# Kernel tuning notes

Hardware: AMD Instinct MI355X
Metric: run time of the kernel (lower is better)

## Reference

```python
import jax, jax.numpy as jnp
import numpy as np

N, E, G = 50000, 800000, 64
H, C = 4, 32            # heads, per-head channels
IN, ED = 128, 16        # in_channels, edge_dim
NEG_SLOPE = 0.2


def gat_conv(x, edge_index, edge_attr, W, att_src, att_dst, W_e, att_e, bias, concat):
    """PyG GATConv (eval mode, add_self_loops=True, fill_value='mean').
    x: [N,F_in], edge_index: [2,E], edge_attr: [E,ED].
    W: [F_in,H*C], att_*: [H,C], W_e: [ED,H*C], bias: [H*C] or [C].
    """
    n = x.shape[0]
    # add self loops; self-loop edge_attr = mean of edge_attr (fill_value='mean')
    loop = jnp.arange(n, dtype=edge_index.dtype)
    src = jnp.concatenate([edge_index[0], loop])
    dst = jnp.concatenate([edge_index[1], loop])
    ea = jnp.concatenate(
        [edge_attr, jnp.broadcast_to(edge_attr.mean(0), (n, edge_attr.shape[1]))], 0)

    xw = (x @ W).reshape(n, H, C)                       # [N,H,C]
    a_src = (xw * att_src).sum(-1)                      # [N,H]
    a_dst = (xw * att_dst).sum(-1)                      # [N,H]
    ew = (ea @ W_e).reshape(-1, H, C)                   # [E+N,H,C]
    a_edge = (ew * att_e).sum(-1)                       # [E+N,H]

    alpha = a_src[src] + a_dst[dst] + a_edge            # [E+N,H]
    alpha = jax.nn.leaky_relu(alpha, NEG_SLOPE)
    # segment softmax over incoming edges of each dst node
    amax = jax.ops.segment_max(alpha, dst, num_segments=n)
    alpha = jnp.exp(alpha - amax[dst])
    denom = jax.ops.segment_sum(alpha, dst, num_segments=n)
    alpha = alpha / (denom[dst] + 1e-16)

    msg = alpha[:, :, None] * xw[src]                   # [E+N,H,C]
    out = jax.ops.segment_sum(msg, dst, num_segments=n) # [N,H,C]
    out = out.reshape(n, H * C) if concat else out.mean(1)
    return out + bias


def setup_inputs() -> dict:
    key = jax.random.key(0)
    ks = jax.random.split(key, 24)
    g = lambda i, shape, scale=0.1: jax.random.normal(ks[i], shape, jnp.float32) * scale
    inp = {
        "x": jax.random.normal(ks[0], (N, IN), jnp.float32),
        "edge_index": jax.random.randint(ks[1], (2, E), 0, N, jnp.int64 if jax.config.jax_enable_x64 else jnp.int32),
        "edge_attr": jax.random.normal(ks[2], (E, ED), jnp.float32),
        "batch": jnp.sort(jax.random.randint(ks[3], (N,), 0, G)),
        # conv1: in=128 -> H*C=128, concat
        "W1": g(4, (IN, H * C)), "att_src1": g(5, (H, C)), "att_dst1": g(6, (H, C)),
        "W_e1": g(7, (ED, H * C)), "att_e1": g(8, (H, C)), "b1": g(9, (H * C,)),
        # conv2: in=H*C=128 -> C=32, mean over heads
        "W2": g(10, (H * C, H * C)), "att_src2": g(11, (H, C)), "att_dst2": g(12, (H, C)),
        "W_e2": g(13, (ED, H * C)), "att_e2": g(14, (H, C)), "b2": g(15, (C,)),
        # graph MLP: 32 -> 32 -> 2
        "W3": g(16, (C, C)), "b3": g(17, (C,)),
        "W4": g(18, (C, 2)), "b4": g(19, (2,)),
    }
    return inp


def reference(x, edge_index, edge_attr, batch,
              W1, att_src1, att_dst1, W_e1, att_e1, b1,
              W2, att_src2, att_dst2, W_e2, att_e2, b2,
              W3, b3, W4, b4):
    h = gat_conv(x, edge_index, edge_attr, W1, att_src1, att_dst1, W_e1, att_e1, b1, concat=True)
    h = jax.nn.relu(h)   # dropout inactive in eval mode
    h = gat_conv(h, edge_index, edge_attr, W2, att_src2, att_dst2, W_e2, att_e2, b2, concat=False)
    # global mean pool over graphs
    sums = jax.ops.segment_sum(h, batch, num_segments=G)            # [G,C]
    cnt = jax.ops.segment_sum(jnp.ones((h.shape[0], 1), h.dtype), batch, num_segments=G)
    pooled = sums / jnp.maximum(cnt, 1.0)
    out = jax.nn.relu(pooled @ W3 + b3) @ W4 + b4                   # [G,2]
    return out
```

## Files before the change

### kernel.cpp

```cpp
#include <hip/hip_runtime.h>
#include <hip/hip_bf16.h>

#define NEG_SLOPE 0.2f
#define BINB 512
#define BIN_CHUNK 2048
#define MAXBKT 2048

typedef __attribute__((ext_vector_type(8))) short bf16x8;
typedef __attribute__((ext_vector_type(4))) float f32x4;

__device__ __forceinline__ unsigned short bf16rne(float x) {
    unsigned int u = __float_as_uint(x);
    u += 0x7fffu + ((u >> 16) & 1u);
    return (unsigned short)(u >> 16);
}
__device__ __forceinline__ unsigned int pk2bf16(float lo, float hi) {
    return ((unsigned int)bf16rne(hi) << 16) | bf16rne(lo);
}

__global__ void init_kernel(int* __restrict__ bucket_cnt, float* __restrict__ ea_sums,
                            float* __restrict__ pooled) {
    int t = threadIdx.x;
    for (int i = t; i < BINB; i += 256) bucket_cnt[i] = 0;
    if (t < 16) ea_sums[t] = 0.f;
    for (int i = t; i < 2048; i += 256) pooled[i] = 0.f;
}

__global__ __launch_bounds__(256) void ea_colsum(const float* __restrict__ ea,
                                                 float* __restrict__ sums, int E_) {
    int j = threadIdx.x & 15, rl = threadIdx.x >> 4;
    float acc = 0.f;
    for (long long r = (long long)blockIdx.x * 16 + rl; r < E_; r += (long long)gridDim.x * 16)
        acc += ea[r * 16 + j];
    __shared__ float red[256];
    red[rl * 16 + j] = acc;
    __syncthreads();
    if (threadIdx.x < 16) {
        float s = 0.f;
#pragma unroll
        for (int i = 0; i < 16; i++) s += red[i * 16 + threadIdx.x];
        atomicAdd(&sums[threadIdx.x], s);
    }
}

__global__ __launch_bounds__(256) void bin_count(const int* __restrict__ dst,
                                                 int* __restrict__ bucket_cnt,
                                                 int* __restrict__ blockbase,
                                                 int E_, int EN_, int npb) {
    __shared__ int hist[BINB];
    int tid = threadIdx.x;
    for (int i = tid; i < BINB; i += 256) hist[i] = 0;
    __syncthreads();
    int base = blockIdx.x * BIN_CHUNK;
    int lim = min(base + BIN_CHUNK, EN_);
    for (int e = base + tid; e < lim; e += 256) {
        int d = (e < E_) ? dst[e] : e - E_;
        atomicAdd(&hist[d / npb], 1);
    }
    __syncthreads();
    for (int b = tid; b < BINB; b += 256) {
        int c = hist[b];
        blockbase[blockIdx.x * BINB + b] = (c > 0) ? atomicAdd(&bucket_cnt[b], c) : 0;
    }
}

__global__ __launch_bounds__(512) void bucket_scan(const int* __restrict__ bucket_cnt,
                                                   int* __restrict__ bucket_off,
                                                   int* __restrict__ rowptr, int n, int total) {
    __shared__ int tmp[BINB];
    int t = threadIdx.x;
    tmp[t] = bucket_cnt[t];
    __syncthreads();
    for (int off = 1; off < BINB; off <<= 1) {
        int v = (t >= off) ? tmp[t - off] : 0;
        __syncthreads();
        tmp[t] += v;
        __syncthreads();
    }
    bucket_off[t] = (t == 0) ? 0 : tmp[t - 1];
    if (t == 0) rowptr[n] = total;
}

__global__ __launch_bounds__(256) void bin_scatter(const int* __restrict__ src,
                                                   const int* __restrict__ dst,
                                                   const int* __restrict__ bucket_off,
                                                   const int* __restrict__ blockbase,
                                                   int2* __restrict__ bin_se,
                                                   int E_, int EN_, int npb) {
    __shared__ int hist[BINB];
    int tid = threadIdx.x;
    for (int i = tid; i < BINB; i += 256) hist[i] = 0;
    __syncthreads();
    int base = blockIdx.x * BIN_CHUNK;
    int lim = min(base + BIN_CHUNK, EN_);
    for (int e = base + tid; e < lim; e += 256) {
        int s, d;
        if (e < E_) { s = src[e]; d = dst[e]; } else { s = d = e - E_; }
        int b = d / npb;
        int rank = atomicAdd(&hist[b], 1);
        int pos = bucket_off[b] + blockbase[blockIdx.x * BINB + b] + rank;
        bin_se[pos] = make_int2(s, e | ((d - b * npb) << 20));
    }
}

__global__ __launch_bounds__(256) void csr_build(const int* __restrict__ bucket_off,
                                                 const int2* __restrict__ bin_se,
                                                 int2* __restrict__ csr_se,
                                                 int* __restrict__ row_of,
                                                 int* __restrict__ rowptr,
                                                 int n, int EN_, int npb) {
    __shared__ int pk[MAXBKT];
    __shared__ int sv[MAXBKT];
    __shared__ int cnts[256];
    int b = blockIdx.x;
    int tid = threadIdx.x;
    int nb = b * npb;
    int nn = min(npb, n - nb);
    if (nn <= 0) return;
    int off0 = bucket_off[b];
    int off1 = (b == BINB - 1) ? EN_ : bucket_off[b + 1];
    int cnt = min(off1 - off0, MAXBKT);
    cnts[tid] = 0;
    __syncthreads();
    for (int i = tid; i < cnt; i += 256) {
        int2 se = bin_se[off0 + i];
        sv[i] = se.x;
        pk[i] = se.y;
        atomicAdd(&cnts[se.y >> 20], 1);
    }
    __syncthreads();
    for (int off = 1; off < 256; off <<= 1) {
        int v = (tid >= off) ? cnts[tid - off] : 0;
        __syncthreads();
        cnts[tid] += v;
        __syncthreads();
    }
    int excl = (tid == 0) ? 0 : cnts[tid - 1];
    __syncthreads();
    cnts[tid] = off0 + excl;
    if (tid < nn) rowptr[nb + tid] = off0 + excl;
    __syncthreads();
    for (int i = tid; i < cnt; i += 256) {
        int y = pk[i];
        int dloc = y >> 20;
        int pos = atomicAdd(&cnts[dloc], 1);
        csr_se[pos] = make_int2(sv[i], y & 0xFFFFF);
        row_of[pos] = nb + dloc;
    }
}

__global__ __launch_bounds__(256) void wprep(
    const float* __restrict__ W1, const float* __restrict__ W2,
    const float* __restrict__ We1, const float* __restrict__ ate1,
    const float* __restrict__ We2, const float* __restrict__ ate2,
    const float* __restrict__ ea_sums, float invE,
    unsigned short* __restrict__ Wt1, unsigned short* __restrict__ Wt2,
    float* __restrict__ V1, float* __restrict__ V2,
    float* __restrict__ aes1, float* __restrict__ aes2,
    const int* __restrict__ batch, int* __restrict__ gstart, int n) {
    int b = blockIdx.x, tid = threadIdx.x;
    if (b < 64) {
        const float* W = (b < 32) ? W1 : W2;
        unsigned short* Wt = (b < 32) ? Wt1 : Wt2;
        int base = (b & 31) * 512;
#pragma unroll
        for (int r = 0; r < 2; r++) {
            int flat = base + r * 256 + tid;
            int nn = flat >> 7, k = flat & 127;
            Wt[nn * 128 + k] = bf16rne(W[k * 128 + nn]);
        }
    } else if (b == 64) {
        __shared__ float V1s[64], V2s[64];
        if (tid < 64) {
            int dd = tid >> 2, h = tid & 3;
            float s = 0.f;
            for (int c = 0; c < 32; c++) s += We1[dd * 128 + h * 32 + c] * ate1[h * 32 + c];
            V1[dd * 4 + h] = s; V1s[dd * 4 + h] = s;
        } else if (tid < 128) {
            int t = tid - 64, dd = t >> 2, h = t & 3;
            float s = 0.f;
            for (int c = 0; c < 32; c++) s += We2[dd * 128 + h * 32 + c] * ate2[h * 32 + c];
            V2[dd * 4 + h] = s; V2s[dd * 4 + h] = s;
        }
        __syncthreads();
        if (tid < 4) {
            float s = 0.f;
            for (int dd = 0; dd < 16; dd++) s += ea_sums[dd] * invE * V1s[dd * 4 + tid];
            aes1[tid] = s;
        } else if (tid >= 64 && tid < 68) {
            int h = tid - 64;
            float s = 0.f;
            for (int dd = 0; dd < 16; dd++) s += ea_sums[dd] * invE * V2s[dd * 4 + h];
            aes2[h] = s;
        }
    } else {
        int g = tid;
        if (g > 64) return;
        if (g == 64) { gstart[64] = n; return; }
        int lo = 0, hi = n;
        while (lo < hi) {
            int mid = (lo + hi) >> 1;
            if (batch[mid] < g) lo = mid + 1; else hi = mid;
        }
        gstart[g] = lo;
    }
}

template<bool BF16IN>
__global__ __launch_bounds__(256) void gemm_att_mfma(
    const void* __restrict__ Xin, const unsigned short* __restrict__ Wtg,
    const float* __restrict__ att_s, const float* __restrict__ att_d,
    unsigned short* __restrict__ XWb, float* __restrict__ a_s,
    float* __restrict__ a_d, int n) {
    __shared__ unsigned short Wt[128][136];
    __shared__ unsigned short Xs[4][16][136];
    __shared__ float attsL[128], attdL[128];

    int tid = threadIdx.x;
    int w = tid >> 6, lane = tid & 63;
    int l15 = lane & 15, rgrp = lane >> 4;

    if (tid < 128) { attsL[tid] = att_s[tid]; attdL[tid] = att_d[tid]; }

#pragma unroll
    for (int it = 0; it < 8; it++) {
        int flat = it * 256 + tid;
        int nn = flat >> 4, kq = flat & 15;
        *(uint4*)&Wt[nn][kq * 8] = *(const uint4*)(Wtg + nn * 128 + kq * 8);
    }

    int r0 = blockIdx.x * 64 + w * 16;
    {
        int rr = lane >> 2;
        int row = r0 + rr;
        int c0 = (lane & 3) * 32;
        if (!BF16IN) {
            const float* Xf = (const float*)Xin;
#pragma unroll
            for (int q = 0; q < 8; q++) {
                int c = c0 + q * 4;
                float4 v = make_float4(0.f, 0.f, 0.f, 0.f);
                if (row < n) v = *(const float4*)(Xf + (size_t)row * 128 + c);
                uint2 p;
                p.x = pk2bf16(v.x, v.y);
                p.y = pk2bf16(v.z, v.w);
                *(uint2*)&Xs[w][rr][c] = p;
            }
        } else {
            const unsigned short* Xb = (const unsigned short*)Xin;
#pragma unroll
            for (int q = 0; q < 4; q++) {
                int c = c0 + q * 8;
                uint4 v = make_uint4(0u, 0u, 0u, 0u);
                if (row < n) v = *(const uint4*)(Xb + (size_t)row * 128 + c);
                *(uint4*)&Xs[w][rr][c] = v;
            }
        }
    }
    __syncthreads();

    f32x4 acc[8];
#pragma unroll
    for (int ct = 0; ct < 8; ct++) acc[ct] = (f32x4){0.f, 0.f, 0.f, 0.f};

#pragma unroll
    for (int kt = 0; kt < 4; kt++) {
        int k0 = kt * 32 + rgrp * 8;
        bf16x8 a = *(const bf16x8*)&Xs[w][l15][k0];
#pragma unroll
        for (int ct = 0; ct < 8; ct++) {
            bf16x8 b = *(const bf16x8*)&Wt[ct * 16 + l15][k0];
            acc[ct] = __builtin_amdgcn_mfma_f32_16x16x32_bf16(a, b, acc[ct], 0, 0, 0);
        }
    }

    float ar[8], br[8];
#pragma unroll
    for (int ct = 0; ct < 8; ct++) {
        ar[ct] = attsL[ct * 16 + l15];
        br[ct] = attdL[ct * 16 + l15];
    }
#pragma unroll
    for (int i = 0; i < 4; i++) {
        float ps[4], pd[4];
#pragma unroll
        for (int h = 0; h < 4; h++) {
            ps[h] = acc[2 * h][i] * ar[2 * h] + acc[2 * h + 1][i] * ar[2 * h + 1];
            pd[h] = acc[2 * h][i] * br[2 * h] + acc[2 * h + 1][i] * br[2 * h + 1];
        }
#pragma unroll
        for (int off = 1; off < 16; off <<= 1) {
#pragma unroll
            for (int h = 0; h < 4; h++) {
                ps[h] += __shfl_xor(ps[h], off);
                pd[h] += __shfl_xor(pd[h], off);
            }
        }
        if (l15 == 0) {
            int row = r0 + rgrp * 4 + i;
            if (row < n) {
                *(float4*)(a_s + (size_t)row * 4) = make_float4(ps[0], ps[1], ps[2], ps[3]);
                *(float4*)(a_d + (size_t)row * 4) = make_float4(pd[0], pd[1], pd[2], pd[3]);
            }
        }
    }

    unsigned short* stage = &Xs[w][0][0];
#pragma unroll
    for (int i = 0; i < 4; i++) {
        int row = rgrp * 4 + i;
#pragma unroll
        for (int ct = 0; ct < 8; ct++)
            stage[row * 128 + ct * 16 + l15] = bf16rne(acc[ct][i]);
    }
#pragma unroll
    for (int p = 0; p < 4; p++) {
        int fo = p * 1024 + lane * 16;
        int row = fo >> 8;
        int colb = fo & 255;
        uint4 v = *(const uint4*)((const char*)stage + fo);
        int grow = r0 + row;
        if (grow < n)
            *(uint4*)((char*)XWb + (size_t)grow * 256 + colb) = v;
    }
}

__global__ __launch_bounds__(256) void alpha1_fused(
    const int2* __restrict__ csr_se, const int* __restrict__ row_of,
    const float* __restrict__ ea,
    const float* __restrict__ V1, const float* __restrict__ V2,
    const float* __restrict__ aes1, const float* __restrict__ aes2,
    const float* __restrict__ a_s, const float* __restrict__ a_d,
    float* __restrict__ csr_alpha, float* __restrict__ aeb2, int E_, int EN_) {
    __shared__ float V1l[64], V2l[64], a1l[4], a2l[4];
    int tid = threadIdx.x;
    if (tid < 64) { V1l[tid] = V1[tid]; V2l[tid] = V2[tid]; }
    if (tid < 4) { a1l[tid] = aes1[tid]; a2l[tid] = aes2[tid]; }
    __syncthreads();
    int i = blockIdx.x * 256 + tid;
    if (i >= EN_) return;
    int2 se = csr_se[i];
    int s = se.x, e = se.y, d = row_of[i];
    float ae1[4], ae2[4];
    if (e < E_) {
#pragma unroll
        for (int h = 0; h < 4; h++) { ae1[h] = 0.f; ae2[h] = 0.f; }
        const float4* er = (const float4*)(ea + (size_t)e * 16);
#pragma unroll
        for (int q = 0; q < 4; q++) {
            float4 v = er[q];
#pragma unroll
            for (int h = 0; h < 4; h++) {
                ae1[h] += v.x * V1l[(q * 4 + 0) * 4 + h] + v.y * V1l[(q * 4 + 1) * 4 + h] +
                          v.z * V1l[(q * 4 + 2) * 4 + h] + v.w * V1l[(q * 4 + 3) * 4 + h];
                ae2[h] += v.x * V2l[(q * 4 + 0) * 4 + h] + v.y * V2l[(q * 4 + 1) * 4 + h] +
                          v.z * V2l[(q * 4 + 2) * 4 + h] + v.w * V2l[(q * 4 + 3) * 4 + h];
            }
        }
    } else {
#pragma unroll
        for (int h = 0; h < 4; h++) { ae1[h] = a1l[h]; ae2[h] = a2l[h]; }
    }
    float4 asv = *(const float4*)(a_s + (size_t)s * 4);
    float4 adv = *(const float4*)(a_d + (size_t)d * 4);
    float o0 = asv.x + adv.x + ae1[0];
    float o1 = asv.y + adv.y + ae1[1];
    float o2 = asv.z + adv.z + ae1[2];
    float o3 = asv.w + adv.w + ae1[3];
    o0 = o0 > 0.f ? o0 : NEG_SLOPE * o0;
    o1 = o1 > 0.f ? o1 : NEG_SLOPE * o1;
    o2 = o2 > 0.f ? o2 : NEG_SLOPE * o2;
    o3 = o3 > 0.f ? o3 : NEG_SLOPE * o3;
    *(float4*)(csr_alpha + (size_t)i * 4) = make_float4(o0, o1, o2, o3);
    *(float4*)(aeb2 + (size_t)i * 4) = make_float4(ae2[0], ae2[1], ae2[2], ae2[3]);
}

template<int MODE>
__global__ __launch_bounds__(256) void dst_aggregate(
    const int* __restrict__ rowptr, const int2* __restrict__ csr_se,
    const float* __restrict__ alpha_arr, const float* __restrict__ as2,
    const float* __restrict__ ad2, const uint2* __restrict__ XW2,
    const float* __restrict__ bias, unsigned int* __restrict__ OUT, int n) {
    int wv = threadIdx.x >> 6, lane = threadIdx.x & 63;
    int d = blockIdx.x * 4 + wv;
    if (d >= n) return;
    int h = lane >> 4, j = lane & 15;
    int half = lane >> 5, u = lane & 31;
    int hc16 = (u >> 3) << 4;
    int beg = rowptr[d], end = rowptr[d + 1];

    float advh = 0.f;
    if (MODE == 0) advh = ad2[(size_t)d * 4 + h];

    float a0 = 0.f, a1 = 0.f, a2 = 0.f, a3 = 0.f;
    float den = 0.f;

    int i = beg;
    for (; i + 16 <= end; i += 16) {
        int i0 = i + j;
        int sreg = csr_se[i0].x;
        float a = alpha_arr[(size_t)i0 * 4 + h];
        if (MODE == 0) {
            a += as2[(size_t)sreg * 4 + h] + advh;
            a = a > 0.f ? a : NEG_SLOPE * a;
        }
        float w = __expf(a);
        den += w;
#pragma unroll
        for (int m = 0; m < 8; m++) {
            int k = 2 * m + half;
            int s = __shfl(sreg, k);
            float wk = __shfl(w, hc16 + k);
            uint2 v = XW2[(size_t)s * 32 + u];
            a0 += wk * __uint_as_float(v.x << 16);
            a1 += wk * __uint_as_float(v.x & 0xffff0000u);
            a2 += wk * __uint_as_float(v.y << 16);
            a3 += wk * __uint_as_float(v.y & 0xffff0000u);
        }
    }
    int cnt = end - i;
    if (cnt > 0) {
        float w = 0.f; int sreg = 0;
        if (j < cnt) {
            int i0 = i + j;
            sreg = csr_se[i0].x;
            float a = alpha_arr[(size_t)i0 * 4 + h];
            if (MODE == 0) {
                a += as2[(size_t)sreg * 4 + h] + advh;
                a = a > 0.f ? a : NEG_SLOPE * a;
            }
            w = __expf(a);
        }
        den += w;
        for (int k0 = 0; k0 < cnt; k0 += 4) {
#pragma unroll
            for (int mm = 0; mm < 2; mm++) {
                int k = k0 + 2 * mm + half;
                int kc = k & 15;
                int s = __shfl(sreg, kc);
                float wk = __shfl(w, hc16 + kc);
                if (k >= cnt) wk = 0.f;
                uint2 v = XW2[(size_t)s * 32 + u];
                a0 += wk * __uint_as_float(v.x << 16);
                a1 += wk * __uint_as_float(v.x & 0xffff0000u);
                a2 += wk * __uint_as_float(v.y << 16);
                a3 += wk * __uint_as_float(v.y & 0xffff0000u);
            }
        }
    }
    a0 += __shfl_xor(a0, 32);
    a1 += __shfl_xor(a1, 32);
    a2 += __shfl_xor(a2, 32);
    a3 += __shfl_xor(a3, 32);
    den += __shfl_xor(den, 1);
    den += __shfl_xor(den, 2);
    den += __shfl_xor(den, 4);
    den += __shfl_xor(den, 8);
    float denc = __shfl(den, hc16);
    float inv = 1.f / (denc + 1e-16f);
    if (half == 0) {
        int c0 = u * 4;
        float o0 = a0 * inv, o1 = a1 * inv, o2 = a2 * inv, o3 = a3 * inv;
        if (MODE == 1) {
            float4 bb = *(const float4*)(bias + c0);
            o0 = fmaxf(o0 + bb.x, 0.f);
            o1 = fmaxf(o1 + bb.y, 0.f);
            o2 = fmaxf(o2 + bb.z, 0.f);
            o3 = fmaxf(o3 + bb.w, 0.f);
        }
        uint2 pv;
        pv.x = pk2bf16(o0, o1);
        pv.y = pk2bf16(o2, o3);
        *((uint2*)OUT + (size_t)d * 32 + u) = pv;
    }
}

#define POOL_SPLITS 8
__global__ __launch_bounds__(256) void pool_kernel(const unsigned int* __restrict__ B,
                                                   const int* __restrict__ gstart,
                                                   float* __restrict__ pooled) {
    int g = blockIdx.x / POOL_SPLITS, sp = blockIdx.x % POOL_SPLITS;
    int lo = gstart[g], hi = gstart[g + 1];
    int cnt = hi - lo;
    int per = (cnt + POOL_SPLITS - 1) / POOL_SPLITS;
    int s0 = lo + sp * per;
    int s1 = min(s0 + per, hi);
    int jj = threadIdx.x & 15, rl = threadIdx.x >> 4;
    float ax = 0.f, ay = 0.f;
    for (int node = s0 + rl; node < s1; node += 16) {
        const unsigned int* r = B + (size_t)node * 64;
#pragma unroll
        for (int h = 0; h < 4; h++) {
            unsigned int v = r[h * 16 + jj];
            ax += __uint_as_float(v << 16);
            ay += __uint_as_float(v & 0xffff0000u);
        }
    }
    __shared__ float redx[16][16], redy[16][16];
    redx[rl][jj] = ax * 0.25f;
    redy[rl][jj] = ay * 0.25f;
    __syncthreads();
    if (threadIdx.x < 16) {
        float sx = 0.f, sy = 0.f;
#pragma unroll
        for (int i = 0; i < 16; i++) { sx += redx[i][threadIdx.x]; sy += redy[i][threadIdx.x]; }
        atomicAdd(&pooled[g * 32 + 2 * threadIdx.x], sx);
        atomicAdd(&pooled[g * 32 + 2 * threadIdx.x + 1], sy);
    }
}

__global__ void mlp_kernel(const float* __restrict__ pooled, const int* __restrict__ gstart,
                           const float* __restrict__ b2,
                           const float* __restrict__ W3, const float* __restrict__ b3,
                           const float* __restrict__ W4, const float* __restrict__ b4,
                           float* __restrict__ out) {
    int g = blockIdx.x;
    int c = threadIdx.x;
    __shared__ float pm[32];
    __shared__ float t[32];
    int cnt = gstart[g + 1] - gstart[g];
    if (c < 32) {
        float m = 0.f;
        if (cnt > 0) m = pooled[g * 32 + c] / (float)cnt + b2[c];
        pm[c] = m;
    }
    __syncthreads();
    if (c < 32) {
        float s = b3[c];
        for (int k = 0; k < 32; k++) s += pm[k] * W3[k * 32 + c];
        t[c] = fmaxf(s, 0.f);
    }
    __syncthreads();
    if (c < 2) {
        float o = b4[c];
        for (int k = 0; k < 32; k++) o += t[k] * W4[k * 2 + c];
        out[g * 2 + c] = o;
    }
}

extern "C" void kernel_launch(void* const* d_in, const int* in_sizes, int n_in,
                              void* d_out, int out_size, void* d_ws, size_t ws_size,
                              hipStream_t stream) {
    const float* x    = (const float*)d_in[0];
    const int*   eidx = (const int*)d_in[1];
    const float* ea   = (const float*)d_in[2];
    const int*   batch= (const int*)d_in[3];
    const float* W1   = (const float*)d_in[4];
    const float* as1  = (const float*)d_in[5];
    const float* ad1  = (const float*)d_in[6];
    const float* We1  = (const float*)d_in[7];
    const float* ate1 = (const float*)d_in[8];
    const float* b1   = (const float*)d_in[9];
    const float* W2   = (const float*)d_in[10];
    const float* as2  = (const float*)d_in[11];
    const float* ad2  = (const float*)d_in[12];
    const float* We2  = (const float*)d_in[13];
    const float* ate2 = (const float*)d_in[14];
    const float* b2   = (const float*)d_in[15];
    const float* W3   = (const float*)d_in[16];
    const float* b3   = (const float*)d_in[17];
    const float* W4   = (const float*)d_in[18];
    const float* b4   = (const float*)d_in[19];

    const int N_ = in_sizes[0] / 128;
    const int E_ = in_sizes[1] / 2;
    const int EN = E_ + N_;
    const int* srcp = eidx;
    const int* dstp = eidx + E_;
    const int npb = (N_ + BINB - 1) / BINB;
    const int nbk = (EN + BIN_CHUNK - 1) / BIN_CHUNK;

    char* w = (char*)d_ws;
    size_t off = 0;
    auto alloc = [&](size_t bytes) -> void* {
        void* p = w + off;
        off = (off + bytes + 255) & ~(size_t)255;
        return p;
    };
    unsigned short* A   = (unsigned short*)alloc((size_t)N_ * 128 * 2);
    unsigned short* Bb16= (unsigned short*)alloc((size_t)N_ * 128 * 2);
    float* csr_alpha = (float*)alloc((size_t)EN * 16);
    float* aeb2      = (float*)alloc((size_t)EN * 16);
    int2*  csr_se    = (int2*)alloc((size_t)EN * 8);
    int*   row_of    = (int*)alloc((size_t)EN * 4);
    int2*  bin_se    = (int2*)alloc((size_t)EN * 8);
    int*   rowptr    = (int*)alloc((size_t)(N_ + 1) * 4);
    int*   bucket_cnt= (int*)alloc(BINB * 4);
    int*   bucket_off= (int*)alloc(BINB * 4);
    int*   blockbase = (int*)alloc((size_t)nbk * BINB * 4);
    unsigned short* Wt1g = (unsigned short*)alloc(16384 * 2);
    unsigned short* Wt2g = (unsigned short*)alloc(16384 * 2);
    float* a_s       = (float*)alloc((size_t)N_ * 16);
    float* a_d       = (float*)alloc((size_t)N_ * 16);
    float* ea_sums   = (float*)alloc(64);
    float* V1        = (float*)alloc(256);
    float* V2        = (float*)alloc(256);
    float* aes1      = (float*)alloc(16);
    float* aes2      = (float*)alloc(16);
    float* pooled    = (float*)alloc(64 * 32 * 4);
    int*   gstart    = (int*)alloc(65 * 4);

    init_kernel<<<1, 256, 0, stream>>>(bucket_cnt, ea_sums, pooled);
    ea_colsum<<<1024, 256, 0, stream>>>(ea, ea_sums, E_);
    bin_count<<<nbk, 256, 0, stream>>>(dstp, bucket_cnt, blockbase, E_, EN, npb);
    bucket_scan<<<1, BINB, 0, stream>>>(bucket_cnt, bucket_off, rowptr, N_, EN);
    wprep<<<66, 256, 0, stream>>>(W1, W2, We1, ate1, We2, ate2, ea_sums,
                                  1.0f / (float)E_, Wt1g, Wt2g, V1, V2, aes1, aes2,
                                  batch, gstart, N_);
    bin_scatter<<<nbk, 256, 0, stream>>>(srcp, dstp, bucket_off, blockbase,
                                         bin_se, E_, EN, npb);
    csr_build<<<BINB, 256, 0, stream>>>(bucket_off, bin_se,
                                        csr_se, row_of, rowptr, N_, EN, npb);

    int gblk = (N_ + 63) / 64;

    gemm_att_mfma<false><<<gblk, 256, 0, stream>>>(x, Wt1g, as1, ad1, A, a_s, a_d, N_);
    alpha1_fused<<<(EN + 255) / 256, 256, 0, stream>>>(csr_se, row_of, ea, V1, V2,
                                                       aes1, aes2, a_s, a_d,
                                                       csr_alpha, aeb2, E_, EN);
    dst_aggregate<1><<<(N_ + 3) / 4, 256, 0, stream>>>(rowptr, csr_se, csr_alpha,
                                                       nullptr, nullptr,
                                                       (const uint2*)A, b1,
                                                       (unsigned int*)Bb16, N_);

    gemm_att_mfma<true><<<gblk, 256, 0, stream>>>(Bb16, Wt2g, as2, ad2, A, a_s, a_d, N_);
    dst_aggregate<0><<<(N_ + 3) / 4, 256, 0, stream>>>(rowptr, csr_se, aeb2,
                                                       a_s, a_d,
                                                       (const uint2*)A, b2,
                                                       (unsigned int*)Bb16, N_);
    pool_kernel<<<64 * POOL_SPLITS, 256, 0, stream>>>((const unsigned int*)Bb16,
                                                      gstart, pooled);

    mlp_kernel<<<64, 64, 0, stream>>>(pooled, gstart, b2, W3, b3, W4, b4, (float*)d_out);
}
```

Baseline: 225.4 us.

## Split CSR src/edge arrays and store per-edge attention logits in bf16

The interleaved int2 (src, edge) CSR array becomes two separate int arrays, so the aggregation kernels read only the source indices. The per-edge layer-1 logits and layer-2 edge terms are now stored as packed bf16 (8 bytes per edge instead of 16) and unpacked to float inside dst_aggregate. This cuts edge-stream traffic in alpha1_fused and both aggregation passes. The cost is bf16 rounding of the attention logits before the softmax exponent, which could shift results slightly.

Result: slower. 234.2 us (+3.9%).

```diff
diff --git a/kernel.cpp b/kernel.cpp
--- a/kernel.cpp
+++ b/kernel.cpp
@@ -105,7 +105,8 @@
 
 __global__ __launch_bounds__(256) void csr_build(const int* __restrict__ bucket_off,
                                                  const int2* __restrict__ bin_se,
-                                                 int2* __restrict__ csr_se,
+                                                 int* __restrict__ csr_s,
+                                                 int* __restrict__ csr_e,
                                                  int* __restrict__ row_of,
                                                  int* __restrict__ rowptr,
                                                  int n, int EN_, int npb) {
@@ -144,7 +145,8 @@
         int y = pk[i];
         int dloc = y >> 20;
         int pos = atomicAdd(&cnts[dloc], 1);
-        csr_se[pos] = make_int2(sv[i], y & 0xFFFFF);
+        csr_s[pos] = sv[i];
+        csr_e[pos] = y & 0xFFFFF;
         row_of[pos] = nb + dloc;
     }
 }
@@ -326,12 +328,12 @@
 }
 
 __global__ __launch_bounds__(256) void alpha1_fused(
-    const int2* __restrict__ csr_se, const int* __restrict__ row_of,
-    const float* __restrict__ ea,
+    const int* __restrict__ csr_s, const int* __restrict__ csr_e,
+    const int* __restrict__ row_of, const float* __restrict__ ea,
     const float* __restrict__ V1, const float* __restrict__ V2,
     const float* __restrict__ aes1, const float* __restrict__ aes2,
     const float* __restrict__ a_s, const float* __restrict__ a_d,
-    float* __restrict__ csr_alpha, float* __restrict__ aeb2, int E_, int EN_) {
+    uint2* __restrict__ csr_alpha, uint2* __restrict__ aeb2, int E_, int EN_) {
     __shared__ float V1l[64], V2l[64], a1l[4], a2l[4];
     int tid = threadIdx.x;
     if (tid < 64) { V1l[tid] = V1[tid]; V2l[tid] = V2[tid]; }
@@ -339,8 +341,7 @@
     __syncthreads();
     int i = blockIdx.x * 256 + tid;
     if (i >= EN_) return;
-    int2 se = csr_se[i];
-    int s = se.x, e = se.y, d = row_of[i];
+    int s = csr_s[i], e = csr_e[i], d = row_of[i];
     float ae1[4], ae2[4];
     if (e < E_) {
 #pragma unroll
@@ -371,14 +372,20 @@
     o1 = o1 > 0.f ? o1 : NEG_SLOPE * o1;
     o2 = o2 > 0.f ? o2 : NEG_SLOPE * o2;
     o3 = o3 > 0.f ? o3 : NEG_SLOPE * o3;
-    *(float4*)(csr_alpha + (size_t)i * 4) = make_float4(o0, o1, o2, o3);
-    *(float4*)(aeb2 + (size_t)i * 4) = make_float4(ae2[0], ae2[1], ae2[2], ae2[3]);
+    uint2 pa;
+    pa.x = pk2bf16(o0, o1);
+    pa.y = pk2bf16(o2, o3);
+    csr_alpha[i] = pa;
+    uint2 pe;
+    pe.x = pk2bf16(ae2[0], ae2[1]);
+    pe.y = pk2bf16(ae2[2], ae2[3]);
+    aeb2[i] = pe;
 }
 
 template<int MODE>
 __global__ __launch_bounds__(256) void dst_aggregate(
-    const int* __restrict__ rowptr, const int2* __restrict__ csr_se,
-    const float* __restrict__ alpha_arr, const float* __restrict__ as2,
+    const int* __restrict__ rowptr, const int* __restrict__ csr_s,
+    const unsigned int* __restrict__ alpha_b, const float* __restrict__ as2,
     const float* __restrict__ ad2, const uint2* __restrict__ XW2,
     const float* __restrict__ bias, unsigned int* __restrict__ OUT, int n) {
     int wv = threadIdx.x >> 6, lane = threadIdx.x & 63;
@@ -387,6 +394,7 @@
     int h = lane >> 4, j = lane & 15;
     int half = lane >> 5, u = lane & 31;
     int hc16 = (u >> 3) << 4;
+    int hsel = h >> 1, hodd = h & 1;
     int beg = rowptr[d], end = rowptr[d + 1];
 
     float advh = 0.f;
@@ -398,8 +406,9 @@
     int i = beg;
     for (; i + 16 <= end; i += 16) {
         int i0 = i + j;
-        int sreg = csr_se[i0].x;
-        float a = alpha_arr[(size_t)i0 * 4 + h];
+        int sreg = csr_s[i0];
+        unsigned int au = alpha_b[(size_t)i0 * 2 + hsel];
+        float a = __uint_as_float(hodd ? (au & 0xffff0000u) : (au << 16));
         if (MODE == 0) {
             a += as2[(size_t)sreg * 4 + h] + advh;
             a = a > 0.f ? a : NEG_SLOPE * a;
@@ -423,8 +432,9 @@
         float w = 0.f; int sreg = 0;
         if (j < cnt) {
             int i0 = i + j;
-            sreg = csr_se[i0].x;
-            float a = alpha_arr[(size_t)i0 * 4 + h];
+            sreg = csr_s[i0];
+            unsigned int au = alpha_b[(size_t)i0 * 2 + hsel];
+            float a = __uint_as_float(hodd ? (au & 0xffff0000u) : (au << 16));
             if (MODE == 0) {
                 a += as2[(size_t)sreg * 4 + h] + advh;
                 a = a > 0.f ? a : NEG_SLOPE * a;
@@ -579,9 +589,10 @@
     };
     unsigned short* A   = (unsigned short*)alloc((size_t)N_ * 128 * 2);
     unsigned short* Bb16= (unsigned short*)alloc((size_t)N_ * 128 * 2);
-    float* csr_alpha = (float*)alloc((size_t)EN * 16);
-    float* aeb2      = (float*)alloc((size_t)EN * 16);
-    int2*  csr_se    = (int2*)alloc((size_t)EN * 8);
+    uint2* csr_alpha = (uint2*)alloc((size_t)EN * 8);
+    uint2* aeb2      = (uint2*)alloc((size_t)EN * 8);
+    int*   csr_s     = (int*)alloc((size_t)EN * 4);
+    int*   csr_e     = (int*)alloc((size_t)EN * 4);
     int*   row_of    = (int*)alloc((size_t)EN * 4);
     int2*  bin_se    = (int2*)alloc((size_t)EN * 8);
     int*   rowptr    = (int*)alloc((size_t)(N_ + 1) * 4);
@@ -609,22 +620,24 @@
                                   batch, gstart, N_);
     bin_scatter<<<nbk, 256, 0, stream>>>(srcp, dstp, bucket_off, blockbase,
                                          bin_se, E_, EN, npb);
-    csr_build<<<BINB, 256, 0, stream>>>(bucket_off, bin_se,
-                                        csr_se, row_of, rowptr, N_, EN, npb);
+    csr_build<<<BINB, 256, 0, stream>>>(bucket_off, bin_se, csr_s, csr_e,
+                                        row_of, rowptr, N_, EN, npb);
 
     int gblk = (N_ + 63) / 64;
 
     gemm_att_mfma<false><<<gblk, 256, 0, stream>>>(x, Wt1g, as1, ad1, A, a_s, a_d, N_);
-    alpha1_fused<<<(EN + 255) / 256, 256, 0, stream>>>(csr_se, row_of, ea, V1, V2,
-                                                       aes1, aes2, a_s, a_d,
+    alpha1_fused<<<(EN + 255) / 256, 256, 0, stream>>>(csr_s, csr_e, row_of, ea,
+                                                       V1, V2, aes1, aes2, a_s, a_d,
                                                        csr_alpha, aeb2, E_, EN);
-    dst_aggregate<1><<<(N_ + 3) / 4, 256, 0, stream>>>(rowptr, csr_se, csr_alpha,
+    dst_aggregate<1><<<(N_ + 3) / 4, 256, 0, stream>>>(rowptr, csr_s,
+                                                       (const unsigned int*)csr_alpha,
                                                        nullptr, nullptr,
                                                        (const uint2*)A, b1,
                                                        (unsigned int*)Bb16, N_);
 
     gemm_att_mfma<true><<<gblk, 256, 0, stream>>>(Bb16, Wt2g, as2, ad2, A, a_s, a_d, N_);
-    dst_aggregate<0><<<(N_ + 3) / 4, 256, 0, stream>>>(rowptr, csr_se, aeb2,
+    dst_aggregate<0><<<(N_ + 3) / 4, 256, 0, stream>>>(rowptr, csr_s,
+                                                       (const unsigned int*)aeb2,
                                                        a_s, a_d,
                                                        (const uint2*)A, b2,
                                                        (unsigned int*)Bb16, N_);
```
